# Performance work log

Hardware: AMD Instinct MI355X
Metric: run time of the kernel (lower is better)

The kernel has to match this reference:

```python
import jax, jax.numpy as jnp
import numpy as np

B, S, DM, H = 2, 2048, 1024, 16
D = DM // H  # head dim = 64


def setup_inputs() -> dict:
    key = jax.random.key(0)
    k1, k2, k3, k4, k5 = jax.random.split(key, 5)
    hidden_states = jax.random.normal(k1, (B, S, DM), dtype=jnp.float32)
    attention_mask = jnp.zeros((B, 1, S, S), dtype=jnp.float32)
    position_ids = jnp.broadcast_to(jnp.arange(S, dtype=jnp.int32), (B, S))
    # nn.Linear weights stored as (out, in); x @ W.T
    Wq = jax.random.normal(k2, (DM, DM), dtype=jnp.float32) * 0.02
    Wk = jax.random.normal(k3, (DM, DM), dtype=jnp.float32) * 0.02
    Wv = jax.random.normal(k4, (DM, DM), dtype=jnp.float32) * 0.02
    return {"hidden_states": hidden_states, "attention_mask": attention_mask,
            "position_ids": position_ids, "Wq": Wq, "Wk": Wk, "Wv": Wv}


def _rotate_half(x):
    h = x.shape[-1] // 2
    return jnp.concatenate((-x[..., h:], x[..., :h]), axis=-1)


def _rope_cos_sin(position_ids, dtype):
    # inv_freq: (D/2,)
    inv_freq = 1.0 / (10000.0 ** (jnp.arange(0, D, 2, dtype=jnp.float32) / D))
    # freqs: (B, S, D/2)
    freqs = position_ids.astype(jnp.float32)[:, :, None] * inv_freq[None, None, :]
    emb = jnp.concatenate((freqs, freqs), axis=-1)  # (B, S, D)
    return jnp.cos(emb).astype(dtype), jnp.sin(emb).astype(dtype)


def reference(hidden_states, attention_mask, position_ids, Wq, Wk, Wv):
    def split_heads(x):  # (B,S,DM) -> (B,H,S,D)
        return x.reshape(B, S, H, D).transpose(0, 2, 1, 3)

    q = split_heads(hidden_states @ Wq.T)
    k = split_heads(hidden_states @ Wk.T)
    v = split_heads(hidden_states @ Wv.T)

    q = q * (D ** -0.5)

    cos, sin = _rope_cos_sin(position_ids, q.dtype)
    cos = cos[:, None, :, :]  # unsqueeze head dim -> (B,1,S,D)
    sin = sin[:, None, :, :]
    q = q * cos + _rotate_half(q) * sin
    k = k * cos + _rotate_half(k) * sin

    # (B,H,S,S)
    scores = jnp.einsum('bhqd,bhkd->bhqk', q, k) + attention_mask
    probs = jax.nn.softmax(scores.astype(jnp.float32), axis=-1).astype(q.dtype)
    ctx = jnp.einsum('bhqk,bhkd->bhqd', probs, v)  # (B,H,S,D)
    ctx = ctx.transpose(0, 2, 1, 3).reshape(B, S, DM)
    return ctx
```

## Files before the change

kernel.cpp:

```cpp
#include <hip/hip_runtime.h>
#include <math.h>

#define B  2
#define S  2048
#define DM 1024
#define H  16
#define Dh 64
#define BH (B*H)

typedef short  bf16x8 __attribute__((ext_vector_type(8)));
typedef float  f32x4  __attribute__((ext_vector_type(4)));

__device__ __forceinline__ unsigned short f2bf(float f) {
    unsigned u = __float_as_uint(f);
    u = (u + 0x7fffu + ((u >> 16) & 1u)) >> 16;
    return (unsigned short)u;
}
__device__ __forceinline__ float bf2f(unsigned short h) {
    return __uint_as_float((unsigned)h << 16);
}

__global__ __launch_bounds__(256) void cast_kernel(const float* __restrict__ X,
                                                   const float* __restrict__ Wq,
                                                   const float* __restrict__ Wk,
                                                   const float* __restrict__ Wv,
                                                   unsigned short* __restrict__ Xb,
                                                   unsigned short* __restrict__ Wb) {
    const long c = (long)(blockIdx.x * 256 + threadIdx.x) * 4;
    const float* src;
    unsigned short* dst;
    if (c < 4194304L) {
        src = X + c;  dst = Xb + c;
    } else {
        const long c2 = c - 4194304L;
        const int  wi = (int)(c2 >> 20);
        const long r  = c2 & 1048575L;
        src = (wi == 0 ? Wq : (wi == 1 ? Wk : Wv)) + r;
        dst = Wb + c2;
    }
    const float4 v = *(const float4*)src;
    ushort4 o;
    o.x = f2bf(v.x); o.y = f2bf(v.y); o.z = f2bf(v.z); o.w = f2bf(v.w);
    *(ushort4*)dst = o;
}

__global__ __launch_bounds__(256) void qkv_gemm(const unsigned short* __restrict__ Xb,
                                                const unsigned short* __restrict__ Wb,
                                                unsigned short* __restrict__ Qb,
                                                unsigned short* __restrict__ Kb,
                                                unsigned short* __restrict__ Vb) {
    __shared__ __align__(16) unsigned short As[128 * 32];
    __shared__ __align__(16) unsigned short Bs[128 * 32];

    const int tid  = threadIdx.x;
    const int w    = tid >> 6;
    const int lane = tid & 63;
    const int col  = lane & 15;
    const int quad = lane >> 4;
    const int m0 = blockIdx.x * 128;
    const int n0 = blockIdx.y * 128;
    const int mw = (w & 1) * 64;
    const int nw = (w >> 1) * 64;

    f32x4 acc[4][4] = {};

    for (int k0 = 0; k0 < 1024; k0 += 32) {
        __syncthreads();
        #pragma unroll
        for (int i = 0; i < 2; ++i) {
            const int c   = tid + i * 256;
            const int row = c >> 2;
            const int k8  = (c & 3) * 8;
            *(bf16x8*)&As[c * 8] = *(const bf16x8*)(Xb + (size_t)(m0 + row) * 1024 + k0 + k8);
            *(bf16x8*)&Bs[c * 8] = *(const bf16x8*)(Wb + (size_t)(n0 + row) * 1024 + k0 + k8);
        }
        __syncthreads();

        bf16x8 a[4], bf[4];
        #pragma unroll
        for (int i = 0; i < 4; ++i)
            a[i] = *(const bf16x8*)&As[(mw + i * 16 + col) * 32 + quad * 8];
        #pragma unroll
        for (int j = 0; j < 4; ++j)
            bf[j] = *(const bf16x8*)&Bs[(nw + j * 16 + col) * 32 + quad * 8];
        #pragma unroll
        for (int i = 0; i < 4; ++i)
            #pragma unroll
            for (int j = 0; j < 4; ++j)
                acc[i][j] = __builtin_amdgcn_mfma_f32_16x16x32_bf16(a[i], bf[j], acc[i][j], 0, 0, 0);
    }

    const int wsel = n0 >> 10;
    unsigned short* dp = (wsel == 0) ? Qb : ((wsel == 1) ? Kb : Vb);
    #pragma unroll
    for (int i = 0; i < 4; ++i)
        #pragma unroll
        for (int j = 0; j < 4; ++j)
            #pragma unroll
            for (int r = 0; r < 4; ++r) {
                const int m  = m0 + mw + i * 16 + quad * 4 + r;
                const int n  = n0 + nw + j * 16 + col;
                const int n1 = n & 1023;
                const int hh = n1 >> 6, d = n1 & 63;
                const int bb = m >> 11, ss = m & 2047;
                dp[((size_t)(bb * H + hh) * S + ss) * Dh + d] = f2bf(acc[i][j][r]);
            }
}

__global__ __launch_bounds__(256) void rope_kernel(unsigned short* __restrict__ Q,
                                                   unsigned short* __restrict__ K,
                                                   const int* __restrict__ pos) {
    const int idx = blockIdx.x * 256 + threadIdx.x;
    const int i = idx & 31;
    const int s = (idx >> 5) & (S - 1);
    const int h = (idx >> 16) & (H - 1);
    const int b = idx >> 20;

    const float p   = (float)pos[b * S + s];
    const float inv = exp2f(-(float)i * 0.41524101186092029f);
    float sn, cs;
    sincosf(p * inv, &sn, &cs);

    const size_t base = ((size_t)(b * H + h) * S + s) * Dh;
    const float q0 = bf2f(Q[base + i]), q1 = bf2f(Q[base + i + 32]);
    Q[base + i]      = f2bf((q0 * cs - q1 * sn) * 0.125f);
    Q[base + i + 32] = f2bf((q1 * cs + q0 * sn) * 0.125f);
    const float k0 = bf2f(K[base + i]), k1 = bf2f(K[base + i + 32]);
    K[base + i]      = f2bf(k0 * cs - k1 * sn);
    K[base + i + 32] = f2bf(k1 * cs + k0 * sn);
}

#define KSd 72

__global__ __launch_bounds__(256) void attn_kernel(const unsigned short* __restrict__ Q,
                                                   const unsigned short* __restrict__ K,
                                                   const unsigned short* __restrict__ V,
                                                   const float* __restrict__ mask,
                                                   float* __restrict__ out) {
    __shared__ __align__(16) unsigned short Ks[64 * KSd];
    __shared__ __align__(16) unsigned short Vt[64 * KSd];
    __shared__ __align__(16) unsigned short Ps[4 * 32 * KSd];

    const int tid  = threadIdx.x;
    const int w    = tid >> 6;
    const int lane = tid & 63;
    const int col  = lane & 15;
    const int quad = lane >> 4;
    const int bh   = blockIdx.y;
    const int b    = bh >> 4, h = bh & 15;
    const int q0   = blockIdx.x * 128;
    const int qw   = q0 + w * 32;

    bf16x8 qa[2][2];
    #pragma unroll
    for (int u = 0; u < 2; ++u) {
        const unsigned short* qrow = Q + ((size_t)bh * S + qw + u * 16 + col) * Dh;
        qa[u][0] = *(const bf16x8*)(qrow + quad * 8);
        qa[u][1] = *(const bf16x8*)(qrow + 32 + quad * 8);
    }

    f32x4 o[4][2] = {};
    float m_i[2] = {-INFINITY, -INFINITY};
    float l_i[2] = {0.f, 0.f};
    const float* mbase = mask + (size_t)b * S * S;
    unsigned short* pw = Ps + w * 32 * KSd;

    for (int kt = 0; kt < S / 64; ++kt) {
        __syncthreads();
        #pragma unroll
        for (int cc = 0; cc < 2; ++cc) {
            const int c   = tid + cc * 256;
            const int row = c >> 3;
            const int c8  = (c & 7) * 8;
            const size_t g = ((size_t)bh * S + kt * 64 + row) * Dh + c8;
            *(bf16x8*)&Ks[row * KSd + c8] = *(const bf16x8*)(K + g);
            const bf16x8 vv = *(const bf16x8*)(V + g);
            #pragma unroll
            for (int j = 0; j < 8; ++j) {
                const int d  = c8 + j;
                const int kk = row ^ (((d >> 3) & 7) << 3);
                Vt[d * KSd + kk] = ((const unsigned short*)&vv)[j];
            }
        }
        __syncthreads();

        float4 mv[4][2];
        #pragma unroll
        for (int u = 0; u < 2; ++u)
            #pragma unroll
            for (int f = 0; f < 4; ++f)
                mv[f][u] = *(const float4*)(mbase + (size_t)(qw + u * 16 + col) * S
                                            + kt * 64 + f * 16 + quad * 4);

        f32x4 sc[4][2] = {};
        #pragma unroll
        for (int f = 0; f < 4; ++f) {
            const bf16x8 ka0 = *(const bf16x8*)&Ks[(f * 16 + col) * KSd + quad * 8];
            const bf16x8 ka1 = *(const bf16x8*)&Ks[(f * 16 + col) * KSd + 32 + quad * 8];
            #pragma unroll
            for (int u = 0; u < 2; ++u) {
                sc[f][u] = __builtin_amdgcn_mfma_f32_16x16x32_bf16(ka0, qa[u][0], sc[f][u], 0, 0, 0);
                sc[f][u] = __builtin_amdgcn_mfma_f32_16x16x32_bf16(ka1, qa[u][1], sc[f][u], 0, 0, 0);
            }
        }

        #pragma unroll
        for (int u = 0; u < 2; ++u) {
            #pragma unroll
            for (int f = 0; f < 4; ++f) {
                sc[f][u][0] += mv[f][u].x; sc[f][u][1] += mv[f][u].y;
                sc[f][u][2] += mv[f][u].z; sc[f][u][3] += mv[f][u].w;
            }
            float t = -INFINITY;
            #pragma unroll
            for (int f = 0; f < 4; ++f)
                #pragma unroll
                for (int r = 0; r < 4; ++r) t = fmaxf(t, sc[f][u][r]);
            t = fmaxf(t, __shfl_xor(t, 16, 64));
            t = fmaxf(t, __shfl_xor(t, 32, 64));

            const float mnew = fmaxf(m_i[u], t);
            const float corr = __expf(m_i[u] - mnew);
            m_i[u] = mnew;
            float rs = 0.f;
            #pragma unroll
            for (int f = 0; f < 4; ++f)
                #pragma unroll
                for (int r = 0; r < 4; ++r) {
                    const float pv = __expf(sc[f][u][r] - mnew);
                    sc[f][u][r] = pv;
                    rs += pv;
                }
            rs += __shfl_xor(rs, 16, 64);
            rs += __shfl_xor(rs, 32, 64);
            l_i[u] = l_i[u] * corr + rs;
            #pragma unroll
            for (int g = 0; g < 4; ++g) {
                o[g][u][0] *= corr; o[g][u][1] *= corr;
                o[g][u][2] *= corr; o[g][u][3] *= corr;
            }
            unsigned short* pq = pw + (u * 16 + col) * KSd;
            #pragma unroll
            for (int f = 0; f < 4; ++f) {
                const unsigned v0 = (unsigned)f2bf(sc[f][u][0]) | ((unsigned)f2bf(sc[f][u][1]) << 16);
                const unsigned v1 = (unsigned)f2bf(sc[f][u][2]) | ((unsigned)f2bf(sc[f][u][3]) << 16);
                *(unsigned*)&pq[f * 16 + quad * 4]     = v0;
                *(unsigned*)&pq[f * 16 + quad * 4 + 2] = v1;
            }
        }
        __threadfence_block();

        #pragma unroll
        for (int kc = 0; kc < 2; ++kc) {
            bf16x8 pb[2];
            #pragma unroll
            for (int u = 0; u < 2; ++u)
                pb[u] = *(const bf16x8*)&pw[(u * 16 + col) * KSd + kc * 32 + quad * 8];
            #pragma unroll
            for (int g = 0; g < 4; ++g) {
                const int d  = g * 16 + col;
                const int sw = (((d >> 3) & 7) << 3);
                const bf16x8 va = *(const bf16x8*)&Vt[d * KSd + ((kc * 32 + quad * 8) ^ sw)];
                #pragma unroll
                for (int u = 0; u < 2; ++u)
                    o[g][u] = __builtin_amdgcn_mfma_f32_16x16x32_bf16(va, pb[u], o[g][u], 0, 0, 0);
            }
        }
    }

    #pragma unroll
    for (int u = 0; u < 2; ++u) {
        const float inv = 1.f / l_i[u];
        const int   qg  = qw + u * 16 + col;
        float* op = out + ((size_t)b * S + qg) * DM + h * Dh + quad * 4;
        #pragma unroll
        for (int g = 0; g < 4; ++g) {
            float4 ov;
            ov.x = o[g][u][0] * inv; ov.y = o[g][u][1] * inv;
            ov.z = o[g][u][2] * inv; ov.w = o[g][u][3] * inv;
            *(float4*)(op + g * 16) = ov;
        }
    }
}

extern "C" void kernel_launch(void* const* d_in, const int* in_sizes, int n_in,
                              void* d_out, int out_size, void* d_ws, size_t ws_size,
                              hipStream_t stream) {
    const float* hs   = (const float*)d_in[0];
    const float* mask = (const float*)d_in[1];
    const int*   pos  = (const int*)  d_in[2];
    const float* Wq   = (const float*)d_in[3];
    const float* Wk   = (const float*)d_in[4];
    const float* Wv   = (const float*)d_in[5];
    float* out = (float*)d_out;

    unsigned short* Xb = (unsigned short*)d_ws;
    unsigned short* Wb = Xb + 4194304;
    unsigned short* Qb = Wb + 3145728;
    unsigned short* Kb = Qb + 4194304;
    unsigned short* Vb = Kb + 4194304;

    cast_kernel<<<7168, 256, 0, stream>>>(hs, Wq, Wk, Wv, Xb, Wb);
    qkv_gemm<<<dim3(32, 24), 256, 0, stream>>>(Xb, Wb, Qb, Kb, Vb);
    rope_kernel<<<8192, 256, 0, stream>>>(Qb, Kb, pos);
    attn_kernel<<<dim3(S / 128, BH), 256, 0, stream>>>(Qb, Kb, Vb, mask, out);
}
```

Before: 247.8 us.

## Use direct global-to-LDS loads in QKV GEMM and split attention into 8 waves

```diff
diff --git a/kernel.cpp b/kernel.cpp
--- a/kernel.cpp
+++ b/kernel.cpp
@@ -18,6 +18,13 @@
 }
 __device__ __forceinline__ float bf2f(unsigned short h) {
     return __uint_as_float((unsigned)h << 16);
+}
+
+__device__ __forceinline__ void gload_lds16(const unsigned short* g, unsigned short* l) {
+    __builtin_amdgcn_global_load_lds(
+        (const __attribute__((address_space(1))) unsigned int*)g,
+        (__attribute__((address_space(3))) unsigned int*)l,
+        16, 0, 0);
 }
 
 __global__ __launch_bounds__(256) void cast_kernel(const float* __restrict__ X,
@@ -62,32 +69,35 @@
     const int mw = (w & 1) * 64;
     const int nw = (w >> 1) * 64;
 
+    const int srow = (lane >> 2);
+    const int sk8  = (lane & 3) * 8;
+
     f32x4 acc[4][4] = {};
 
     for (int k0 = 0; k0 < 1024; k0 += 32) {
         __syncthreads();
         #pragma unroll
-        for (int i = 0; i < 2; ++i) {
-            const int c   = tid + i * 256;
-            const int row = c >> 2;
-            const int k8  = (c & 3) * 8;
-            *(bf16x8*)&As[c * 8] = *(const bf16x8*)(Xb + (size_t)(m0 + row) * 1024 + k0 + k8);
-            *(bf16x8*)&Bs[c * 8] = *(const bf16x8*)(Wb + (size_t)(n0 + row) * 1024 + k0 + k8);
-        }
-        __syncthreads();
-
-        bf16x8 a[4], bf[4];
+        for (int it = 0; it < 2; ++it) {
+            const int rbase = w * 16 + it * 64;
+            gload_lds16(Xb + (size_t)(m0 + rbase + srow) * 1024 + k0 + sk8,
+                        &As[rbase * 32]);
+            gload_lds16(Wb + (size_t)(n0 + rbase + srow) * 1024 + k0 + sk8,
+                        &Bs[rbase * 32]);
+        }
+        __syncthreads();
+
+        bf16x8 a[4], bb[4];
         #pragma unroll
         for (int i = 0; i < 4; ++i)
             a[i] = *(const bf16x8*)&As[(mw + i * 16 + col) * 32 + quad * 8];
         #pragma unroll
         for (int j = 0; j < 4; ++j)
-            bf[j] = *(const bf16x8*)&Bs[(nw + j * 16 + col) * 32 + quad * 8];
+            bb[j] = *(const bf16x8*)&Bs[(nw + j * 16 + col) * 32 + quad * 8];
         #pragma unroll
         for (int i = 0; i < 4; ++i)
             #pragma unroll
             for (int j = 0; j < 4; ++j)
-                acc[i][j] = __builtin_amdgcn_mfma_f32_16x16x32_bf16(a[i], bf[j], acc[i][j], 0, 0, 0);
+                acc[i][j] = __builtin_amdgcn_mfma_f32_16x16x32_bf16(a[i], bb[j], acc[i][j], 0, 0, 0);
     }
 
     const int wsel = n0 >> 10;
@@ -102,8 +112,8 @@
                 const int n  = n0 + nw + j * 16 + col;
                 const int n1 = n & 1023;
                 const int hh = n1 >> 6, d = n1 & 63;
-                const int bb = m >> 11, ss = m & 2047;
-                dp[((size_t)(bb * H + hh) * S + ss) * Dh + d] = f2bf(acc[i][j][r]);
+                const int bb2 = m >> 11, ss = m & 2047;
+                dp[((size_t)(bb2 * H + hh) * S + ss) * Dh + d] = f2bf(acc[i][j][r]);
             }
 }
 
@@ -132,14 +142,14 @@
 
 #define KSd 72
 
-__global__ __launch_bounds__(256) void attn_kernel(const unsigned short* __restrict__ Q,
+__global__ __launch_bounds__(512) void attn_kernel(const unsigned short* __restrict__ Q,
                                                    const unsigned short* __restrict__ K,
                                                    const unsigned short* __restrict__ V,
                                                    const float* __restrict__ mask,
                                                    float* __restrict__ out) {
     __shared__ __align__(16) unsigned short Ks[64 * KSd];
     __shared__ __align__(16) unsigned short Vt[64 * KSd];
-    __shared__ __align__(16) unsigned short Ps[4 * 32 * KSd];
+    __shared__ __align__(16) unsigned short Ps[8 * 16 * KSd];
 
     const int tid  = threadIdx.x;
     const int w    = tid >> 6;
@@ -149,137 +159,113 @@
     const int bh   = blockIdx.y;
     const int b    = bh >> 4, h = bh & 15;
     const int q0   = blockIdx.x * 128;
-    const int qw   = q0 + w * 32;
-
-    bf16x8 qa[2][2];
-    #pragma unroll
-    for (int u = 0; u < 2; ++u) {
-        const unsigned short* qrow = Q + ((size_t)bh * S + qw + u * 16 + col) * Dh;
-        qa[u][0] = *(const bf16x8*)(qrow + quad * 8);
-        qa[u][1] = *(const bf16x8*)(qrow + 32 + quad * 8);
-    }
-
-    f32x4 o[4][2] = {};
-    float m_i[2] = {-INFINITY, -INFINITY};
-    float l_i[2] = {0.f, 0.f};
-    const float* mbase = mask + (size_t)b * S * S;
-    unsigned short* pw = Ps + w * 32 * KSd;
+    const int qw   = q0 + w * 16;
+
+    const unsigned short* qrow = Q + ((size_t)bh * S + qw + col) * Dh;
+    const bf16x8 qa0 = *(const bf16x8*)(qrow + quad * 8);
+    const bf16x8 qa1 = *(const bf16x8*)(qrow + 32 + quad * 8);
+
+    f32x4 o[4] = {};
+    float m_i = -INFINITY, l_i = 0.f;
+    const float* mrow = mask + (size_t)b * S * S + (size_t)(qw + col) * S;
+    unsigned short* pw = Ps + w * 16 * KSd;
+
+    const int srow = tid >> 3;
+    const int sc8  = (tid & 7) * 8;
 
     for (int kt = 0; kt < S / 64; ++kt) {
         __syncthreads();
-        #pragma unroll
-        for (int cc = 0; cc < 2; ++cc) {
-            const int c   = tid + cc * 256;
-            const int row = c >> 3;
-            const int c8  = (c & 7) * 8;
-            const size_t g = ((size_t)bh * S + kt * 64 + row) * Dh + c8;
-            *(bf16x8*)&Ks[row * KSd + c8] = *(const bf16x8*)(K + g);
+        {
+            const size_t g = ((size_t)bh * S + kt * 64 + srow) * Dh + sc8;
+            *(bf16x8*)&Ks[srow * KSd + sc8] = *(const bf16x8*)(K + g);
             const bf16x8 vv = *(const bf16x8*)(V + g);
             #pragma unroll
             for (int j = 0; j < 8; ++j) {
-                const int d  = c8 + j;
-                const int kk = row ^ (((d >> 3) & 7) << 3);
+                const int d  = sc8 + j;
+                const int kk = srow ^ (((d >> 3) & 7) << 3);
                 Vt[d * KSd + kk] = ((const unsigned short*)&vv)[j];
             }
         }
         __syncthreads();
 
-        float4 mv[4][2];
-        #pragma unroll
-        for (int u = 0; u < 2; ++u)
-            #pragma unroll
-            for (int f = 0; f < 4; ++f)
-                mv[f][u] = *(const float4*)(mbase + (size_t)(qw + u * 16 + col) * S
-                                            + kt * 64 + f * 16 + quad * 4);
-
-        f32x4 sc[4][2] = {};
+        float4 mv[4];
+        #pragma unroll
+        for (int f = 0; f < 4; ++f)
+            mv[f] = *(const float4*)(mrow + kt * 64 + f * 16 + quad * 4);
+
+        f32x4 sc[4] = {};
         #pragma unroll
         for (int f = 0; f < 4; ++f) {
             const bf16x8 ka0 = *(const bf16x8*)&Ks[(f * 16 + col) * KSd + quad * 8];
             const bf16x8 ka1 = *(const bf16x8*)&Ks[(f * 16 + col) * KSd + 32 + quad * 8];
-            #pragma unroll
-            for (int u = 0; u < 2; ++u) {
-                sc[f][u] = __builtin_amdgcn_mfma_f32_16x16x32_bf16(ka0, qa[u][0], sc[f][u], 0, 0, 0);
-                sc[f][u] = __builtin_amdgcn_mfma_f32_16x16x32_bf16(ka1, qa[u][1], sc[f][u], 0, 0, 0);
-            }
-        }
-
-        #pragma unroll
-        for (int u = 0; u < 2; ++u) {
-            #pragma unroll
-            for (int f = 0; f < 4; ++f) {
-                sc[f][u][0] += mv[f][u].x; sc[f][u][1] += mv[f][u].y;
-                sc[f][u][2] += mv[f][u].z; sc[f][u][3] += mv[f][u].w;
-            }
-            float t = -INFINITY;
-            #pragma unroll
-            for (int f = 0; f < 4; ++f)
-                #pragma unroll
-                for (int r = 0; r < 4; ++r) t = fmaxf(t, sc[f][u][r]);
-            t = fmaxf(t, __shfl_xor(t, 16, 64));
-            t = fmaxf(t, __shfl_xor(t, 32, 64));
-
-            const float mnew = fmaxf(m_i[u], t);
-            const float corr = __expf(m_i[u] - mnew);
-            m_i[u] = mnew;
-            float rs = 0.f;
-            #pragma unroll
-            for (int f = 0; f < 4; ++f)
-                #pragma unroll
-                for (int r = 0; r < 4; ++r) {
-                    const float pv = __expf(sc[f][u][r] - mnew);
-                    sc[f][u][r] = pv;
-                    rs += pv;
-                }
-            rs += __shfl_xor(rs, 16, 64);
-            rs += __shfl_xor(rs, 32, 64);
-            l_i[u] = l_i[u] * corr + rs;
-            #pragma unroll
-            for (int g = 0; g < 4; ++g) {
-                o[g][u][0] *= corr; o[g][u][1] *= corr;
-                o[g][u][2] *= corr; o[g][u][3] *= corr;
-            }
-            unsigned short* pq = pw + (u * 16 + col) * KSd;
-            #pragma unroll
-            for (int f = 0; f < 4; ++f) {
-                const unsigned v0 = (unsigned)f2bf(sc[f][u][0]) | ((unsigned)f2bf(sc[f][u][1]) << 16);
-                const unsigned v1 = (unsigned)f2bf(sc[f][u][2]) | ((unsigned)f2bf(sc[f][u][3]) << 16);
-                *(unsigned*)&pq[f * 16 + quad * 4]     = v0;
-                *(unsigned*)&pq[f * 16 + quad * 4 + 2] = v1;
-            }
+            sc[f] = __builtin_amdgcn_mfma_f32_16x16x32_bf16(ka0, qa0, sc[f], 0, 0, 0);
+            sc[f] = __builtin_amdgcn_mfma_f32_16x16x32_bf16(ka1, qa1, sc[f], 0, 0, 0);
+        }
+
+        #pragma unroll
+        for (int f = 0; f < 4; ++f) {
+            sc[f][0] += mv[f].x; sc[f][1] += mv[f].y;
+            sc[f][2] += mv[f].z; sc[f][3] += mv[f].w;
+        }
+        float t = -INFINITY;
+        #pragma unroll
+        for (int f = 0; f < 4; ++f)
+            #pragma unroll
+            for (int r = 0; r < 4; ++r) t = fmaxf(t, sc[f][r]);
+        t = fmaxf(t, __shfl_xor(t, 16, 64));
+        t = fmaxf(t, __shfl_xor(t, 32, 64));
+
+        const float mnew = fmaxf(m_i, t);
+        const float corr = __expf(m_i - mnew);
+        m_i = mnew;
+        float rs = 0.f;
+        #pragma unroll
+        for (int f = 0; f < 4; ++f)
+            #pragma unroll
+            for (int r = 0; r < 4; ++r) {
+                const float pv = __expf(sc[f][r] - mnew);
+                sc[f][r] = pv;
+                rs += pv;
+            }
+        rs += __shfl_xor(rs, 16, 64);
+        rs += __shfl_xor(rs, 32, 64);
+        l_i = l_i * corr + rs;
+        #pragma unroll
+        for (int g = 0; g < 4; ++g) {
+            o[g][0] *= corr; o[g][1] *= corr; o[g][2] *= corr; o[g][3] *= corr;
+        }
+
+        unsigned short* pq = pw + col * KSd;
+        #pragma unroll
+        for (int f = 0; f < 4; ++f) {
+            const unsigned v0 = (unsigned)f2bf(sc[f][0]) | ((unsigned)f2bf(sc[f][1]) << 16);
+            const unsigned v1 = (unsigned)f2bf(sc[f][2]) | ((unsigned)f2bf(sc[f][3]) << 16);
+            *(unsigned*)&pq[f * 16 + quad * 4]     = v0;
+            *(unsigned*)&pq[f * 16 + quad * 4 + 2] = v1;
         }
         __threadfence_block();
 
         #pragma unroll
         for (int kc = 0; kc < 2; ++kc) {
-            bf16x8 pb[2];
-            #pragma unroll
-            for (int u = 0; u < 2; ++u)
-                pb[u] = *(const bf16x8*)&pw[(u * 16 + col) * KSd + kc * 32 + quad * 8];
+            const bf16x8 pb = *(const bf16x8*)&pw[col * KSd + kc * 32 + quad * 8];
             #pragma unroll
             for (int g = 0; g < 4; ++g) {
                 const int d  = g * 16 + col;
                 const int sw = (((d >> 3) & 7) << 3);
                 const bf16x8 va = *(const bf16x8*)&Vt[d * KSd + ((kc * 32 + quad * 8) ^ sw)];
-                #pragma unroll
-                for (int u = 0; u < 2; ++u)
-                    o[g][u] = __builtin_amdgcn_mfma_f32_16x16x32_bf16(va, pb[u], o[g][u], 0, 0, 0);
-            }
-        }
-    }
-
+                o[g] = __builtin_amdgcn_mfma_f32_16x16x32_bf16(va, pb, o[g], 0, 0, 0);
+            }
+        }
+    }
+
+    const float inv = 1.f / l_i;
+    float* op = out + ((size_t)b * S + qw + col) * DM + h * Dh + quad * 4;
     #pragma unroll
-    for (int u = 0; u < 2; ++u) {
-        const float inv = 1.f / l_i[u];
-        const int   qg  = qw + u * 16 + col;
-        float* op = out + ((size_t)b * S + qg) * DM + h * Dh + quad * 4;
-        #pragma unroll
-        for (int g = 0; g < 4; ++g) {
-            float4 ov;
-            ov.x = o[g][u][0] * inv; ov.y = o[g][u][1] * inv;
-            ov.z = o[g][u][2] * inv; ov.w = o[g][u][3] * inv;
-            *(float4*)(op + g * 16) = ov;
-        }
+    for (int g = 0; g < 4; ++g) {
+        float4 ov;
+        ov.x = o[g][0] * inv; ov.y = o[g][1] * inv;
+        ov.z = o[g][2] * inv; ov.w = o[g][3] * inv;
+        *(float4*)(op + g * 16) = ov;
     }
 }
 
@@ -303,5 +289,5 @@
     cast_kernel<<<7168, 256, 0, stream>>>(hs, Wq, Wk, Wv, Xb, Wb);
     qkv_gemm<<<dim3(32, 24), 256, 0, stream>>>(Xb, Wb, Qb, Kb, Vb);
     rope_kernel<<<8192, 256, 0, stream>>>(Qb, Kb, pos);
-    attn_kernel<<<dim3(S / 128, BH), 256, 0, stream>>>(Qb, Kb, Vb, mask, out);
-}
+    attn_kernel<<<dim3(S / 128, BH), 512, 0, stream>>>(Qb, Kb, Vb, mask, out);
+}
```

Result: no change. 243.1 us (-1.9%).
